# Optimization experiments

Measured on AMD Instinct MI355X. Metric: run time of the kernel, lower is better.

## Reference

```python
import jax, jax.numpy as jnp
import numpy as np

D_MODEL = 768
D_STATE = 16
D_CONV = 4
EXPAND = 2
D_INNER = EXPAND * D_MODEL
DT_RANK = (D_MODEL + 15) // 16  # 48
BATCH = 2
SEQ = 1024
LN_EPS = 1e-5


def setup_inputs() -> dict:
    key = jax.random.key(0)
    ks = jax.random.split(key, 12)
    s = 0.02
    inp = {
        "x": jax.random.normal(ks[0], (BATCH, SEQ, D_MODEL), dtype=jnp.float32),
        "in_proj_w": jax.random.normal(ks[1], (2 * D_INNER, D_MODEL), dtype=jnp.float32) * s,
        "conv_w": jax.random.normal(ks[2], (D_INNER, D_CONV), dtype=jnp.float32) * s,
        "conv_b": jnp.zeros((D_INNER,), dtype=jnp.float32),
        "x_proj_w": jax.random.normal(ks[3], (DT_RANK + 2 * D_STATE, D_INNER), dtype=jnp.float32) * s,
        "dt_proj_w": jax.random.normal(ks[4], (D_INNER, DT_RANK), dtype=jnp.float32) * s,
        "dt_proj_b": jnp.full((D_INNER,), -4.0, dtype=jnp.float32),  # softplus(-4) ~ small dt
        "A_log": jnp.log(jnp.broadcast_to(jnp.arange(1, D_STATE + 1, dtype=jnp.float32), (D_INNER, D_STATE))),
        "D": jnp.ones((D_INNER,), dtype=jnp.float32),
        "out_proj_w": jax.random.normal(ks[5], (D_MODEL, D_INNER), dtype=jnp.float32) * s,
        "ln_w": jnp.ones((D_MODEL,), dtype=jnp.float32),
        "ln_b": jnp.zeros((D_MODEL,), dtype=jnp.float32),
    }
    return inp


def _mamba(x, in_proj_w, conv_w, conv_b, x_proj_w, dt_proj_w, dt_proj_b, A_log, D, out_proj_w):
    B, L, _ = x.shape
    # input projection -> [B, L, 2*D_INNER], split into x-branch and gate z
    xz = jnp.einsum("bld,ed->ble", x, in_proj_w)
    xb, z = jnp.split(xz, 2, axis=-1)
    # causal depthwise conv1d along L
    lhs = jnp.transpose(xb, (0, 2, 1))  # [B, D_INNER, L]
    rhs = conv_w[:, None, :]  # [D_INNER, 1, D_CONV]
    xc = jax.lax.conv_general_dilated(
        lhs, rhs, window_strides=(1,), padding=[(D_CONV - 1, 0)],
        dimension_numbers=("NCH", "OIH", "NCH"), feature_group_count=D_INNER)
    xc = jnp.transpose(xc, (0, 2, 1)) + conv_b  # [B, L, D_INNER]
    xc = jax.nn.silu(xc)
    # data-dependent SSM parameters
    x_dbl = jnp.einsum("bld,ed->ble", xc, x_proj_w)  # [B, L, DT_RANK+2*D_STATE]
    dt, Bm, Cm = jnp.split(x_dbl, [DT_RANK, DT_RANK + D_STATE], axis=-1)
    dt = jax.nn.softplus(jnp.einsum("blr,dr->bld", dt, dt_proj_w) + dt_proj_b)  # [B, L, D_INNER]
    A = -jnp.exp(A_log)  # [D_INNER, D_STATE]

    # selective scan over time
    def step(h, inp):
        dt_t, B_t, C_t, u_t = inp  # [B,D_INNER], [B,D_STATE], [B,D_STATE], [B,D_INNER]
        dA = jnp.exp(dt_t[:, :, None] * A)  # [B, D_INNER, D_STATE]
        h = h * dA + (dt_t * u_t)[:, :, None] * B_t[:, None, :]
        y = jnp.einsum("bds,bs->bd", h, C_t)
        return h, y

    h0 = jnp.zeros((B, D_INNER, D_STATE), dtype=x.dtype)
    xs = (jnp.transpose(dt, (1, 0, 2)), jnp.transpose(Bm, (1, 0, 2)),
          jnp.transpose(Cm, (1, 0, 2)), jnp.transpose(xc, (1, 0, 2)))
    _, ys = jax.lax.scan(step, h0, xs)  # ys: [L, B, D_INNER]
    y = jnp.transpose(ys, (1, 0, 2)) + xc * D
    y = y * jax.nn.silu(z)
    return jnp.einsum("ble,de->bld", y, out_proj_w)  # [B, L, D_MODEL]


def reference(x, in_proj_w, conv_w, conv_b, x_proj_w, dt_proj_w, dt_proj_b,
              A_log, D, out_proj_w, ln_w, ln_b):
    residual = x
    h = _mamba(x, in_proj_w, conv_w, conv_b, x_proj_w, dt_proj_w, dt_proj_b, A_log, D, out_proj_w)
    # dropout is identity in eval mode
    y = h + residual
    mu = jnp.mean(y, axis=-1, keepdims=True)
    var = jnp.mean(jnp.square(y - mu), axis=-1, keepdims=True)
    return (y - mu) * jax.lax.rsqrt(var + LN_EPS) * ln_w + ln_b
```

## Files before the change

### kernel.cpp

```cpp
#include <hip/hip_runtime.h>
#include <hip/hip_bf16.h>
#include <math.h>

#define BATCH   2
#define SEQ     1024
#define DMODEL  768
#define DINNER  1536
#define DSTATE  16
#define DTRANK  48
#define NTOK    (BATCH*SEQ)
#define XPROJ_N (DTRANK + 2*DSTATE)

#define LC      32
#define NC      (SEQ/LC)

#define KSPL_IN   2
#define KSPL_OUT  4

typedef unsigned short ushort_t;
typedef __attribute__((ext_vector_type(8))) short bf16x8;
typedef __attribute__((ext_vector_type(4))) float f32x4;

__device__ __forceinline__ ushort_t f2bf(float f) {
    unsigned int u = __float_as_uint(f);
    u += 0x7FFF + ((u >> 16) & 1);
    return (ushort_t)(u >> 16);
}

__global__ __launch_bounds__(256)
void f2b_3(const float* __restrict__ s0, ushort_t* __restrict__ d0, int n0,
           const float* __restrict__ s1, ushort_t* __restrict__ d1, int n1,
           const float* __restrict__ s2, ushort_t* __restrict__ d2, int n2)
{
    const int i = (blockIdx.x * 256 + threadIdx.x) * 4;
    const float* s; ushort_t* d;
    if (i < n0)               { s = s0 + i;            d = d0 + i; }
    else if (i < n0 + n1)     { s = s1 + (i - n0);     d = d1 + (i - n0); }
    else if (i < n0 + n1 + n2){ s = s2 + (i - n0 - n1);d = d2 + (i - n0 - n1); }
    else return;
    const float4 v = *reinterpret_cast<const float4*>(s);
    ushort4 o;
    o.x = f2bf(v.x); o.y = f2bf(v.y); o.z = f2bf(v.z); o.w = f2bf(v.w);
    *reinterpret_cast<ushort4*>(d) = o;
}

#define GLOAD_LDS16(gp, lp) \
    __builtin_amdgcn_global_load_lds((const __attribute__((address_space(1))) void*)(gp), \
                                     (__attribute__((address_space(3))) void*)(lp), 16, 0, 0)

__global__ __launch_bounds__(256)
void gemm_mfma_bt_sk(const ushort_t* __restrict__ A, const ushort_t* __restrict__ W,
                     float* __restrict__ C, int M, int N, int K, int klen)
{
    __shared__ ushort_t As[128 * 32];
    __shared__ ushort_t Bs[128 * 32];

    const int tid  = threadIdx.x;
    const int w    = tid >> 6;
    const int lane = tid & 63;
    const int m0 = blockIdx.y * 128;
    const int n0 = blockIdx.x * 128;
    const int kbeg = blockIdx.z * klen;
    float* Cp = C + (size_t)blockIdx.z * M * N;

    const int lrow = lane >> 2;
    const int lcol = (lane & 3) * 8;

    const ushort_t* ga0 = A + (size_t)(m0 + w * 16 + lrow) * K + kbeg + lcol;
    const ushort_t* ga1 = ga0 + (size_t)64 * K;
    const ushort_t* gb0 = W + (size_t)(n0 + w * 16 + lrow) * K + kbeg + lcol;
    const ushort_t* gb1 = gb0 + (size_t)64 * K;

    ushort_t* lA0 = As + w * 512;
    ushort_t* lA1 = As + 64 * 32 + w * 512;
    ushort_t* lB0 = Bs + w * 512;
    ushort_t* lB1 = Bs + 64 * 32 + w * 512;

    const int wm = w >> 1, wn = w & 1;
    const int fr = lane & 15;
    const int kg = lane >> 4;

    f32x4 acc[4][4] = {};

    for (int kt = 0; kt < klen; kt += 32) {
        __syncthreads();
        GLOAD_LDS16(ga0 + kt, lA0);
        GLOAD_LDS16(ga1 + kt, lA1);
        GLOAD_LDS16(gb0 + kt, lB0);
        GLOAD_LDS16(gb1 + kt, lB1);
        __syncthreads();

        bf16x8 af[4], bfr[4];
        #pragma unroll
        for (int i = 0; i < 4; ++i) {
            af[i]  = *reinterpret_cast<const bf16x8*>(&As[(wm * 64 + i * 16 + fr) * 32 + kg * 8]);
            bfr[i] = *reinterpret_cast<const bf16x8*>(&Bs[(wn * 64 + i * 16 + fr) * 32 + kg * 8]);
        }
        #pragma unroll
        for (int i = 0; i < 4; ++i)
            #pragma unroll
            for (int j = 0; j < 4; ++j)
                acc[i][j] = __builtin_amdgcn_mfma_f32_16x16x32_bf16(af[i], bfr[j], acc[i][j], 0, 0, 0);
    }

    #pragma unroll
    for (int i = 0; i < 4; ++i) {
        const int row_base = m0 + wm * 64 + i * 16 + kg * 4;
        #pragma unroll
        for (int j = 0; j < 4; ++j) {
            const int col = n0 + wn * 64 + j * 16 + fr;
            #pragma unroll
            for (int r = 0; r < 4; ++r)
                Cp[(size_t)(row_base + r) * N + col] = acc[i][j][r];
        }
    }
}

#define BM 64
#define BN 64
#define BK 16

template<int ACT>
__global__ __launch_bounds__(256)
void gemm_tn(const float* __restrict__ A, const float* __restrict__ W,
             const float* __restrict__ bias, float* __restrict__ C,
             int M, int N, int K, int lda)
{
    __shared__ float As[BK][BM + 4];
    __shared__ float Ws[BK][BN + 4];

    const int t  = threadIdx.x;
    const int tx = t & 15;
    const int ty = t >> 4;
    const int row0 = blockIdx.y * BM;
    const int col0 = blockIdx.x * BN;

    const int m_l = t >> 2;
    const int k_l = (t & 3) * 4;

    float acc[4][4] = {};

    for (int kt = 0; kt < K; kt += BK) {
        float4 av, wv;
        {
            const float* ap = A + (size_t)(row0 + m_l) * lda + kt + k_l;
            av = *reinterpret_cast<const float4*>(ap);
        }
        {
            const int wn = col0 + m_l;
            if (wn < N) {
                const float* wp = W + (size_t)wn * K + kt + k_l;
                wv = *reinterpret_cast<const float4*>(wp);
            } else {
                wv = make_float4(0.f, 0.f, 0.f, 0.f);
            }
        }
        __syncthreads();
        As[k_l + 0][m_l] = av.x; As[k_l + 1][m_l] = av.y;
        As[k_l + 2][m_l] = av.z; As[k_l + 3][m_l] = av.w;
        Ws[k_l + 0][m_l] = wv.x; Ws[k_l + 1][m_l] = wv.y;
        Ws[k_l + 2][m_l] = wv.z; Ws[k_l + 3][m_l] = wv.w;
        __syncthreads();

        #pragma unroll
        for (int k = 0; k < BK; ++k) {
            float4 a4 = *reinterpret_cast<const float4*>(&As[k][ty * 4]);
            float4 w4 = *reinterpret_cast<const float4*>(&Ws[k][tx * 4]);
            float af[4] = {a4.x, a4.y, a4.z, a4.w};
            float wf[4] = {w4.x, w4.y, w4.z, w4.w};
            #pragma unroll
            for (int i = 0; i < 4; ++i)
                #pragma unroll
                for (int j = 0; j < 4; ++j)
                    acc[i][j] += af[i] * wf[j];
        }
    }

    #pragma unroll
    for (int i = 0; i < 4; ++i) {
        const int m = row0 + ty * 4 + i;
        #pragma unroll
        for (int j = 0; j < 4; ++j) {
            const int n = col0 + tx * 4 + j;
            if (n < N) {
                float v = acc[i][j];
                if (ACT == 1) {
                    v += bias[n];
                    v = (v > 20.f) ? v : log1pf(expf(v));
                }
                C[(size_t)m * N + n] = v;
            }
        }
    }
}

__global__ __launch_bounds__(256)
void gemm_tn_splitk(const float* __restrict__ A, const float* __restrict__ W,
                    float* __restrict__ C, int M, int N, int K, int lda, int kchunk)
{
    __shared__ float As[BK][BM + 4];
    __shared__ float Ws[BK][BN + 4];

    const int t  = threadIdx.x;
    const int tx = t & 15;
    const int ty = t >> 4;
    const int row0 = blockIdx.y * BM;
    const int col0 = blockIdx.x * BN;
    const int kbeg = blockIdx.z * kchunk;
    const int kend = kbeg + kchunk;

    const int m_l = t >> 2;
    const int k_l = (t & 3) * 4;

    float acc[4][4] = {};

    for (int kt = kbeg; kt < kend; kt += BK) {
        float4 av, wv;
        {
            const float* ap = A + (size_t)(row0 + m_l) * lda + kt + k_l;
            av = *reinterpret_cast<const float4*>(ap);
        }
        {
            const int wn = col0 + m_l;
            if (wn < N) {
                const float* wp = W + (size_t)wn * K + kt + k_l;
                wv = *reinterpret_cast<const float4*>(wp);
            } else {
                wv = make_float4(0.f, 0.f, 0.f, 0.f);
            }
        }
        __syncthreads();
        As[k_l + 0][m_l] = av.x; As[k_l + 1][m_l] = av.y;
        As[k_l + 2][m_l] = av.z; As[k_l + 3][m_l] = av.w;
        Ws[k_l + 0][m_l] = wv.x; Ws[k_l + 1][m_l] = wv.y;
        Ws[k_l + 2][m_l] = wv.z; Ws[k_l + 3][m_l] = wv.w;
        __syncthreads();

        #pragma unroll
        for (int k = 0; k < BK; ++k) {
            float4 a4 = *reinterpret_cast<const float4*>(&As[k][ty * 4]);
            float4 w4 = *reinterpret_cast<const float4*>(&Ws[k][tx * 4]);
            float af[4] = {a4.x, a4.y, a4.z, a4.w};
            float wf[4] = {w4.x, w4.y, w4.z, w4.w};
            #pragma unroll
            for (int i = 0; i < 4; ++i)
                #pragma unroll
                for (int j = 0; j < 4; ++j)
                    acc[i][j] += af[i] * wf[j];
        }
    }

    #pragma unroll
    for (int i = 0; i < 4; ++i) {
        const int m = row0 + ty * 4 + i;
        #pragma unroll
        for (int j = 0; j < 4; ++j) {
            const int n = col0 + tx * 4 + j;
            if (n < N)
                atomicAdd(&C[(size_t)m * N + n], acc[i][j]);
        }
    }
}

__global__ __launch_bounds__(256)
void conv_silu(const float* __restrict__ xzA, const float* __restrict__ xzB,
               const float* __restrict__ cw, const float* __restrict__ cb,
               float* __restrict__ xc)
{
    int idx = blockIdx.x * 256 + threadIdx.x;
    if (idx >= NTOK * DINNER) return;
    const int c = idx % DINNER;
    const int m = idx / DINNER;
    const int l = m & (SEQ - 1);

    const float w0 = cw[c * 4 + 0], w1 = cw[c * 4 + 1],
                w2 = cw[c * 4 + 2], w3 = cw[c * 4 + 3];
    const float* a = xzA + (size_t)m * (2 * DINNER) + c;
    const float* b = xzB + (size_t)m * (2 * DINNER) + c;
    const int R = 2 * DINNER;

    float acc = cb[c] + (a[0] + b[0]) * w3;
    if (l >= 1) acc += (a[-R]     + b[-R])     * w2;
    if (l >= 2) acc += (a[-2 * R] + b[-2 * R]) * w1;
    if (l >= 3) acc += (a[-3 * R] + b[-3 * R]) * w0;

    const float sig = 1.f / (1.f + __expf(-acc));
    xc[idx] = acc * sig;
}

__global__ __launch_bounds__(256)
void scan_chunk_state(const float* __restrict__ dt, const float* __restrict__ xc,
                      const float* __restrict__ xdbl, const float* __restrict__ A_log,
                      float* __restrict__ hA, float* __restrict__ aP)
{
    __shared__ float B_s[LC * 16];

    const int c  = blockIdx.x;
    const int d0 = blockIdx.y * 256;
    const int b  = blockIdx.z;
    const int t  = threadIdx.x;
    const int d  = d0 + t;

    const size_t row0 = (size_t)b * SEQ + (size_t)c * LC;

    #pragma unroll
    for (int p = 0; p < (LC * 16) / 256; ++p) {
        const int idx = p * 256 + t;
        const int l = idx >> 4, j = idx & 15;
        B_s[idx] = xdbl[(row0 + l) * XPROJ_N + DTRANK + j];
    }
    __syncthreads();

    float Aval[16];
    #pragma unroll
    for (int q = 0; q < 4; ++q) {
        const float4 a4 = *reinterpret_cast<const float4*>(&A_log[(size_t)d * DSTATE + q * 4]);
        Aval[q*4+0] = -expf(a4.x); Aval[q*4+1] = -expf(a4.y);
        Aval[q*4+2] = -expf(a4.z); Aval[q*4+3] = -expf(a4.w);
    }

    float h[16];
    #pragma unroll
    for (int s = 0; s < 16; ++s) h[s] = 0.f;
    float dts = 0.f;

    #pragma unroll 2
    for (int l = 0; l < LC; ++l) {
        const size_t m = row0 + l;
        const float dtv = dt[m * DINNER + d];
        const float u   = xc[m * DINNER + d];
        const float du  = dtv * u;
        dts += dtv;
        float Bv[16];
        #pragma unroll
        for (int q = 0; q < 4; ++q) {
            const float4 b4 = *reinterpret_cast<const float4*>(&B_s[l * 16 + q * 4]);
            Bv[q*4+0] = b4.x; Bv[q*4+1] = b4.y; Bv[q*4+2] = b4.z; Bv[q*4+3] = b4.w;
        }
        #pragma unroll
        for (int s = 0; s < 16; ++s)
            h[s] = h[s] * __expf(dtv * Aval[s]) + du * Bv[s];
    }

    const size_t o = (((size_t)(b * NC + c) * DINNER) + d) * DSTATE;
    #pragma unroll
    for (int q = 0; q < 4; ++q) {
        float4 hv = make_float4(h[q*4+0], h[q*4+1], h[q*4+2], h[q*4+3]);
        float4 pv = make_float4(__expf(Aval[q*4+0]*dts), __expf(Aval[q*4+1]*dts),
                                __expf(Aval[q*4+2]*dts), __expf(Aval[q*4+3]*dts));
        *reinterpret_cast<float4*>(&hA[o + q*4]) = hv;
        *reinterpret_cast<float4*>(&aP[o + q*4]) = pv;
    }
}

__global__ __launch_bounds__(256)
void scan_combine(float* __restrict__ hA, const float* __restrict__ aP)
{
    const int idx = blockIdx.x * 256 + threadIdx.x;
    const int b  = idx / (DINNER * DSTATE);
    const int ds = idx % (DINNER * DSTATE);

    float h = 0.f;
    #pragma unroll
    for (int c = 0; c < NC; ++c) {
        const size_t o = ((size_t)(b * NC + c) * DINNER * DSTATE) + ds;
        const float a = hA[o];
        const float p = aP[o];
        hA[o] = h;
        h = a + h * p;
    }
}

__global__ __launch_bounds__(256)
void scan_apply(const float* __restrict__ dt, const float* __restrict__ xc,
                const float* __restrict__ xdbl,
                const float* __restrict__ xzA, const float* __restrict__ xzB,
                const float* __restrict__ A_log, const float* __restrict__ Dp,
                const float* __restrict__ hInit, ushort_t* __restrict__ y)
{
    __shared__ float B_s[LC * 16];
    __shared__ float C_s[LC * 16];

    const int c  = blockIdx.x;
    const int d0 = blockIdx.y * 256;
    const int b  = blockIdx.z;
    const int t  = threadIdx.x;
    const int d  = d0 + t;

    const size_t row0 = (size_t)b * SEQ + (size_t)c * LC;

    #pragma unroll
    for (int p = 0; p < (LC * 16) / 256; ++p) {
        const int idx = p * 256 + t;
        const int l = idx >> 4, j = idx & 15;
        B_s[idx] = xdbl[(row0 + l) * XPROJ_N + DTRANK + j];
        C_s[idx] = xdbl[(row0 + l) * XPROJ_N + DTRANK + DSTATE + j];
    }
    __syncthreads();

    float Aval[16];
    #pragma unroll
    for (int q = 0; q < 4; ++q) {
        const float4 a4 = *reinterpret_cast<const float4*>(&A_log[(size_t)d * DSTATE + q * 4]);
        Aval[q*4+0] = -expf(a4.x); Aval[q*4+1] = -expf(a4.y);
        Aval[q*4+2] = -expf(a4.z); Aval[q*4+3] = -expf(a4.w);
    }
    const float Dd = Dp[d];

    const size_t o = (((size_t)(b * NC + c) * DINNER) + d) * DSTATE;
    float h[16];
    #pragma unroll
    for (int q = 0; q < 4; ++q) {
        const float4 h4 = *reinterpret_cast<const float4*>(&hInit[o + q*4]);
        h[q*4+0] = h4.x; h[q*4+1] = h4.y; h[q*4+2] = h4.z; h[q*4+3] = h4.w;
    }

    #pragma unroll 2
    for (int l = 0; l < LC; ++l) {
        const size_t m = row0 + l;
        const float dtv = dt[m * DINNER + d];
        const float u   = xc[m * DINNER + d];
        const size_t zi = m * (2 * DINNER) + DINNER + d;
        const float zv  = xzA[zi] + xzB[zi];
        const float du  = dtv * u;

        float acc = 0.f;
        #pragma unroll
        for (int q = 0; q < 4; ++q) {
            const float4 b4 = *reinterpret_cast<const float4*>(&B_s[l * 16 + q * 4]);
            const float4 c4 = *reinterpret_cast<const float4*>(&C_s[l * 16 + q * 4]);
            const float bb[4] = {b4.x, b4.y, b4.z, b4.w};
            const float cc[4] = {c4.x, c4.y, c4.z, c4.w};
            #pragma unroll
            for (int r = 0; r < 4; ++r) {
                const int s = q * 4 + r;
                h[s] = h[s] * __expf(dtv * Aval[s]) + du * bb[r];
                acc += h[s] * cc[r];
            }
        }

        const float yv  = acc + u * Dd;
        const float sig = 1.f / (1.f + __expf(-zv));
        y[m * DINNER + d] = f2bf(yv * zv * sig);
    }
}

__global__ __launch_bounds__(256)
void ln_kernel(const float* __restrict__ mo, const float* __restrict__ x,
               const float* __restrict__ w, const float* __restrict__ bias,
               float* __restrict__ out)
{
    const int m = blockIdx.x;
    const int t = threadIdx.x;
    const size_t MN = (size_t)NTOK * DMODEL;
    const float* mrow = mo + (size_t)m * DMODEL;
    const float* xrow = x  + (size_t)m * DMODEL;

    float v[3];
    float sum = 0.f, ss = 0.f;
    #pragma unroll
    for (int i = 0; i < 3; ++i) {
        const int col = t + 256 * i;
        float acc = xrow[col];
        #pragma unroll
        for (int p = 0; p < KSPL_OUT; ++p)
            acc += mrow[p * MN + col];
        v[i] = acc;
        sum += acc;
        ss  += acc * acc;
    }
    #pragma unroll
    for (int o = 1; o < 64; o <<= 1) {
        sum += __shfl_xor(sum, o);
        ss  += __shfl_xor(ss, o);
    }
    __shared__ float red[2][4];
    const int wid = t >> 6;
    if ((t & 63) == 0) { red[0][wid] = sum; red[1][wid] = ss; }
    __syncthreads();
    sum = red[0][0] + red[0][1] + red[0][2] + red[0][3];
    ss  = red[1][0] + red[1][1] + red[1][2] + red[1][3];

    const float mu   = sum * (1.f / DMODEL);
    const float var  = ss * (1.f / DMODEL) - mu * mu;
    const float rstd = rsqrtf(var + 1e-5f);

    #pragma unroll
    for (int i = 0; i < 3; ++i) {
        const int col = t + 256 * i;
        out[(size_t)m * DMODEL + col] = (v[i] - mu) * rstd * w[col] + bias[col];
    }
}

extern "C" void kernel_launch(void* const* d_in, const int* in_sizes, int n_in,
                              void* d_out, int out_size, void* d_ws, size_t ws_size,
                              hipStream_t stream)
{
    const float* x          = (const float*)d_in[0];
    const float* in_proj_w  = (const float*)d_in[1];
    const float* conv_w     = (const float*)d_in[2];
    const float* conv_b     = (const float*)d_in[3];
    const float* x_proj_w   = (const float*)d_in[4];
    const float* dt_proj_w  = (const float*)d_in[5];
    const float* dt_proj_b  = (const float*)d_in[6];
    const float* A_log      = (const float*)d_in[7];
    const float* Dp         = (const float*)d_in[8];
    const float* out_proj_w = (const float*)d_in[9];
    const float* ln_w       = (const float*)d_in[10];
    const float* ln_b       = (const float*)d_in[11];
    float* out = (float*)d_out;

    float* ws   = (float*)d_ws;
    float* xz   = ws;
    float* xc   = xz   + (size_t)KSPL_IN * NTOK * 3072;
    float* xdbl = xc   + (size_t)NTOK * 1536;
    float* dt   = xdbl + (size_t)NTOK * 80;
    float* mo   = dt   + (size_t)NTOK * 1536;
    ushort_t* xb16 = (ushort_t*)(mo + (size_t)KSPL_OUT * NTOK * 768);
    ushort_t* ipw16 = xb16  + (size_t)NTOK * DMODEL;
    ushort_t* opw16 = ipw16 + (size_t)2 * DINNER * DMODEL;
    ushort_t* ybb   = opw16 + (size_t)DMODEL * DINNER;

    float* xzA = xz;
    float* xzB = xz + (size_t)NTOK * 3072;

    float* aP = mo;
    float* hA = (float*)d_out;

    {
        const int n0 = NTOK * DMODEL;
        const int n1 = 2 * DINNER * DMODEL;
        const int n2 = DMODEL * DINNER;
        const int nvec = (n0 + n1 + n2) / 4;
        f2b_3<<<(nvec + 255) / 256, 256, 0, stream>>>(
            x, xb16, n0, in_proj_w, ipw16, n1, out_proj_w, opw16, n2);
    }

    gemm_mfma_bt_sk<<<dim3(2 * DINNER / 128, NTOK / 128, KSPL_IN), 256, 0, stream>>>(
        xb16, ipw16, xz, NTOK, 2 * DINNER, DMODEL, DMODEL / KSPL_IN);

    conv_silu<<<(NTOK * DINNER) / 256, 256, 0, stream>>>(xzA, xzB, conv_w, conv_b, xc);

    hipMemsetAsync(xdbl, 0, (size_t)NTOK * XPROJ_N * sizeof(float), stream);
    gemm_tn_splitk<<<dim3((XPROJ_N + BN - 1) / BN, NTOK / BM, 8), 256, 0, stream>>>(
        xc, x_proj_w, xdbl, NTOK, XPROJ_N, DINNER, DINNER, DINNER / 8);

    gemm_tn<1><<<dim3(DINNER / BN, NTOK / BM), 256, 0, stream>>>(
        xdbl, dt_proj_w, dt_proj_b, dt, NTOK, DINNER, DTRANK, XPROJ_N);

    scan_chunk_state<<<dim3(NC, DINNER / 256, BATCH), 256, 0, stream>>>(
        dt, xc, xdbl, A_log, hA, aP);
    scan_combine<<<(BATCH * DINNER * DSTATE) / 256, 256, 0, stream>>>(hA, aP);
    scan_apply<<<dim3(NC, DINNER / 256, BATCH), 256, 0, stream>>>(
        dt, xc, xdbl, xzA, xzB, A_log, Dp, hA, ybb);

    gemm_mfma_bt_sk<<<dim3(DMODEL / 128, NTOK / 128, KSPL_OUT), 256, 0, stream>>>(
        ybb, opw16, mo, NTOK, DMODEL, DINNER, DINNER / KSPL_OUT);

    ln_kernel<<<NTOK, 256, 0, stream>>>(mo, x, ln_w, ln_b, out);
}
```

Before: 257.1 us.

## Replace x_proj atomic split-K with partial buffers, vectorize conv and scan combine

```diff
diff --git a/kernel.cpp b/kernel.cpp
--- a/kernel.cpp
+++ b/kernel.cpp
@@ -10,12 +10,14 @@
 #define DTRANK  48
 #define NTOK    (BATCH*SEQ)
 #define XPROJ_N (DTRANK + 2*DSTATE)
+#define XP_PSZ  ((size_t)NTOK * XPROJ_N)
 
 #define LC      32
 #define NC      (SEQ/LC)
 
 #define KSPL_IN   2
 #define KSPL_OUT  4
+#define KSPL_XP   8
 
 typedef unsigned short ushort_t;
 typedef __attribute__((ext_vector_type(8))) short bf16x8;
@@ -120,27 +122,31 @@
 #define BN 64
 #define BK 16
 
-template<int ACT>
-__global__ __launch_bounds__(256)
-void gemm_tn(const float* __restrict__ A, const float* __restrict__ W,
-             const float* __restrict__ bias, float* __restrict__ C,
-             int M, int N, int K, int lda)
+__global__ __launch_bounds__(256)
+void gemm_tn_xp(const float* __restrict__ A, const float* __restrict__ W,
+                float* __restrict__ C)
 {
     __shared__ float As[BK][BM + 4];
     __shared__ float Ws[BK][BN + 4];
+
+    const int M = NTOK, N = XPROJ_N, K = DINNER, lda = DINNER;
+    const int kchunk = DINNER / KSPL_XP;
 
     const int t  = threadIdx.x;
     const int tx = t & 15;
     const int ty = t >> 4;
     const int row0 = blockIdx.y * BM;
     const int col0 = blockIdx.x * BN;
+    const int kbeg = blockIdx.z * kchunk;
+    const int kend = kbeg + kchunk;
+    float* Cp = C + (size_t)blockIdx.z * XP_PSZ;
 
     const int m_l = t >> 2;
     const int k_l = (t & 3) * 4;
 
     float acc[4][4] = {};
 
-    for (int kt = 0; kt < K; kt += BK) {
+    for (int kt = kbeg; kt < kend; kt += BK) {
         float4 av, wv;
         {
             const float* ap = A + (size_t)(row0 + m_l) * lda + kt + k_l;
@@ -182,52 +188,47 @@
         #pragma unroll
         for (int j = 0; j < 4; ++j) {
             const int n = col0 + tx * 4 + j;
-            if (n < N) {
-                float v = acc[i][j];
-                if (ACT == 1) {
-                    v += bias[n];
-                    v = (v > 20.f) ? v : log1pf(expf(v));
-                }
-                C[(size_t)m * N + n] = v;
-            }
-        }
-    }
-}
-
-__global__ __launch_bounds__(256)
-void gemm_tn_splitk(const float* __restrict__ A, const float* __restrict__ W,
-                    float* __restrict__ C, int M, int N, int K, int lda, int kchunk)
+            if (n < N)
+                Cp[(size_t)m * N + n] = acc[i][j];
+        }
+    }
+}
+
+__global__ __launch_bounds__(256)
+void gemm_tn_dt(const float* __restrict__ Ap, const float* __restrict__ W,
+                const float* __restrict__ bias, float* __restrict__ C)
 {
     __shared__ float As[BK][BM + 4];
     __shared__ float Ws[BK][BN + 4];
+
+    const int N = DINNER, K = DTRANK, lda = XPROJ_N;
 
     const int t  = threadIdx.x;
     const int tx = t & 15;
     const int ty = t >> 4;
     const int row0 = blockIdx.y * BM;
     const int col0 = blockIdx.x * BN;
-    const int kbeg = blockIdx.z * kchunk;
-    const int kend = kbeg + kchunk;
 
     const int m_l = t >> 2;
     const int k_l = (t & 3) * 4;
 
     float acc[4][4] = {};
 
-    for (int kt = kbeg; kt < kend; kt += BK) {
-        float4 av, wv;
+    for (int kt = 0; kt < K; kt += BK) {
+        float4 av = make_float4(0.f, 0.f, 0.f, 0.f);
         {
-            const float* ap = A + (size_t)(row0 + m_l) * lda + kt + k_l;
-            av = *reinterpret_cast<const float4*>(ap);
-        }
+            const size_t off = (size_t)(row0 + m_l) * lda + kt + k_l;
+            #pragma unroll
+            for (int p = 0; p < KSPL_XP; ++p) {
+                const float4 v = *reinterpret_cast<const float4*>(Ap + p * XP_PSZ + off);
+                av.x += v.x; av.y += v.y; av.z += v.z; av.w += v.w;
+            }
+        }
+        float4 wv;
         {
             const int wn = col0 + m_l;
-            if (wn < N) {
-                const float* wp = W + (size_t)wn * K + kt + k_l;
-                wv = *reinterpret_cast<const float4*>(wp);
-            } else {
-                wv = make_float4(0.f, 0.f, 0.f, 0.f);
-            }
+            const float* wp = W + (size_t)wn * K + kt + k_l;
+            wv = *reinterpret_cast<const float4*>(wp);
         }
         __syncthreads();
         As[k_l + 0][m_l] = av.x; As[k_l + 1][m_l] = av.y;
@@ -256,8 +257,9 @@
         #pragma unroll
         for (int j = 0; j < 4; ++j) {
             const int n = col0 + tx * 4 + j;
-            if (n < N)
-                atomicAdd(&C[(size_t)m * N + n], acc[i][j]);
+            float v = acc[i][j] + bias[n];
+            v = (v > 20.f) ? v : log1pf(expf(v));
+            C[(size_t)m * N + n] = v;
         }
     }
 }
@@ -267,30 +269,61 @@
                const float* __restrict__ cw, const float* __restrict__ cb,
                float* __restrict__ xc)
 {
-    int idx = blockIdx.x * 256 + threadIdx.x;
-    if (idx >= NTOK * DINNER) return;
-    const int c = idx % DINNER;
-    const int m = idx / DINNER;
-    const int l = m & (SEQ - 1);
-
-    const float w0 = cw[c * 4 + 0], w1 = cw[c * 4 + 1],
-                w2 = cw[c * 4 + 2], w3 = cw[c * 4 + 3];
-    const float* a = xzA + (size_t)m * (2 * DINNER) + c;
-    const float* b = xzB + (size_t)m * (2 * DINNER) + c;
-    const int R = 2 * DINNER;
-
-    float acc = cb[c] + (a[0] + b[0]) * w3;
-    if (l >= 1) acc += (a[-R]     + b[-R])     * w2;
-    if (l >= 2) acc += (a[-2 * R] + b[-2 * R]) * w1;
-    if (l >= 3) acc += (a[-3 * R] + b[-3 * R]) * w0;
-
-    const float sig = 1.f / (1.f + __expf(-acc));
-    xc[idx] = acc * sig;
+    const int vid = blockIdx.x * 256 + threadIdx.x;
+    const int c4 = (vid % (DINNER / 4)) * 4;
+    const int m  = vid / (DINNER / 4);
+    const int l  = m & (SEQ - 1);
+    const int R  = 2 * DINNER;
+
+    const float* a = xzA + (size_t)m * R + c4;
+    const float* b = xzB + (size_t)m * R + c4;
+
+    float4 W0 = *reinterpret_cast<const float4*>(cw + (c4 + 0) * 4);
+    float4 W1 = *reinterpret_cast<const float4*>(cw + (c4 + 1) * 4);
+    float4 W2 = *reinterpret_cast<const float4*>(cw + (c4 + 2) * 4);
+    float4 W3 = *reinterpret_cast<const float4*>(cw + (c4 + 3) * 4);
+    const float4 bias = *reinterpret_cast<const float4*>(cb + c4);
+
+    float4 s0 = *reinterpret_cast<const float4*>(a);
+    {
+        const float4 t = *reinterpret_cast<const float4*>(b);
+        s0.x += t.x; s0.y += t.y; s0.z += t.z; s0.w += t.w;
+    }
+    float acc0 = bias.x + s0.x * W0.w;
+    float acc1 = bias.y + s0.y * W1.w;
+    float acc2 = bias.z + s0.z * W2.w;
+    float acc3 = bias.w + s0.w * W3.w;
+
+    if (l >= 1) {
+        float4 s = *reinterpret_cast<const float4*>(a - R);
+        const float4 t = *reinterpret_cast<const float4*>(b - R);
+        s.x += t.x; s.y += t.y; s.z += t.z; s.w += t.w;
+        acc0 += s.x * W0.z; acc1 += s.y * W1.z; acc2 += s.z * W2.z; acc3 += s.w * W3.z;
+    }
+    if (l >= 2) {
+        float4 s = *reinterpret_cast<const float4*>(a - 2 * R);
+        const float4 t = *reinterpret_cast<const float4*>(b - 2 * R);
+        s.x += t.x; s.y += t.y; s.z += t.z; s.w += t.w;
+        acc0 += s.x * W0.y; acc1 += s.y * W1.y; acc2 += s.z * W2.y; acc3 += s.w * W3.y;
+    }
+    if (l >= 3) {
+        float4 s = *reinterpret_cast<const float4*>(a - 3 * R);
+        const float4 t = *reinterpret_cast<const float4*>(b - 3 * R);
+        s.x += t.x; s.y += t.y; s.z += t.z; s.w += t.w;
+        acc0 += s.x * W0.x; acc1 += s.y * W1.x; acc2 += s.z * W2.x; acc3 += s.w * W3.x;
+    }
+
+    float4 o;
+    o.x = acc0 / (1.f + __expf(-acc0));
+    o.y = acc1 / (1.f + __expf(-acc1));
+    o.z = acc2 / (1.f + __expf(-acc2));
+    o.w = acc3 / (1.f + __expf(-acc3));
+    *reinterpret_cast<float4*>(xc + (size_t)m * DINNER + c4) = o;
 }
 
 __global__ __launch_bounds__(256)
 void scan_chunk_state(const float* __restrict__ dt, const float* __restrict__ xc,
-                      const float* __restrict__ xdbl, const float* __restrict__ A_log,
+                      const float* __restrict__ xdblP, const float* __restrict__ A_log,
                       float* __restrict__ hA, float* __restrict__ aP)
 {
     __shared__ float B_s[LC * 16];
@@ -307,7 +340,11 @@
     for (int p = 0; p < (LC * 16) / 256; ++p) {
         const int idx = p * 256 + t;
         const int l = idx >> 4, j = idx & 15;
-        B_s[idx] = xdbl[(row0 + l) * XPROJ_N + DTRANK + j];
+        const size_t off = (row0 + l) * XPROJ_N + DTRANK + j;
+        float v = 0.f;
+        #pragma unroll
+        for (int q = 0; q < KSPL_XP; ++q) v += xdblP[q * XP_PSZ + off];
+        B_s[idx] = v;
     }
     __syncthreads();
 
@@ -359,21 +396,27 @@
     const int idx = blockIdx.x * 256 + threadIdx.x;
     const int b  = idx / (DINNER * DSTATE);
     const int ds = idx % (DINNER * DSTATE);
-
+    const size_t stride = (size_t)DINNER * DSTATE;
+    const size_t base = (size_t)b * NC * stride + ds;
+
+    float a[NC], p[NC];
+    #pragma unroll
+    for (int c = 0; c < NC; ++c) {
+        a[c] = hA[base + (size_t)c * stride];
+        p[c] = aP[base + (size_t)c * stride];
+    }
     float h = 0.f;
     #pragma unroll
     for (int c = 0; c < NC; ++c) {
-        const size_t o = ((size_t)(b * NC + c) * DINNER * DSTATE) + ds;
-        const float a = hA[o];
-        const float p = aP[o];
-        hA[o] = h;
-        h = a + h * p;
+        const float hn = a[c] + h * p[c];
+        hA[base + (size_t)c * stride] = h;
+        h = hn;
     }
 }
 
 __global__ __launch_bounds__(256)
 void scan_apply(const float* __restrict__ dt, const float* __restrict__ xc,
-                const float* __restrict__ xdbl,
+                const float* __restrict__ xdblP,
                 const float* __restrict__ xzA, const float* __restrict__ xzB,
                 const float* __restrict__ A_log, const float* __restrict__ Dp,
                 const float* __restrict__ hInit, ushort_t* __restrict__ y)
@@ -393,8 +436,15 @@
     for (int p = 0; p < (LC * 16) / 256; ++p) {
         const int idx = p * 256 + t;
         const int l = idx >> 4, j = idx & 15;
-        B_s[idx] = xdbl[(row0 + l) * XPROJ_N + DTRANK + j];
-        C_s[idx] = xdbl[(row0 + l) * XPROJ_N + DTRANK + DSTATE + j];
+        const size_t offB = (row0 + l) * XPROJ_N + DTRANK + j;
+        float vb = 0.f, vc = 0.f;
+        #pragma unroll
+        for (int q = 0; q < KSPL_XP; ++q) {
+            vb += xdblP[q * XP_PSZ + offB];
+            vc += xdblP[q * XP_PSZ + offB + DSTATE];
+        }
+        B_s[idx] = vb;
+        C_s[idx] = vc;
     }
     __syncthreads();
 
@@ -514,7 +564,7 @@
     float* xz   = ws;
     float* xc   = xz   + (size_t)KSPL_IN * NTOK * 3072;
     float* xdbl = xc   + (size_t)NTOK * 1536;
-    float* dt   = xdbl + (size_t)NTOK * 80;
+    float* dt   = xdbl + (size_t)KSPL_XP * XP_PSZ;
     float* mo   = dt   + (size_t)NTOK * 1536;
     ushort_t* xb16 = (ushort_t*)(mo + (size_t)KSPL_OUT * NTOK * 768);
     ushort_t* ipw16 = xb16  + (size_t)NTOK * DMODEL;
@@ -539,14 +589,13 @@
     gemm_mfma_bt_sk<<<dim3(2 * DINNER / 128, NTOK / 128, KSPL_IN), 256, 0, stream>>>(
         xb16, ipw16, xz, NTOK, 2 * DINNER, DMODEL, DMODEL / KSPL_IN);
 
-    conv_silu<<<(NTOK * DINNER) / 256, 256, 0, stream>>>(xzA, xzB, conv_w, conv_b, xc);
-
-    hipMemsetAsync(xdbl, 0, (size_t)NTOK * XPROJ_N * sizeof(float), stream);
-    gemm_tn_splitk<<<dim3((XPROJ_N + BN - 1) / BN, NTOK / BM, 8), 256, 0, stream>>>(
-        xc, x_proj_w, xdbl, NTOK, XPROJ_N, DINNER, DINNER, DINNER / 8);
-
-    gemm_tn<1><<<dim3(DINNER / BN, NTOK / BM), 256, 0, stream>>>(
-        xdbl, dt_proj_w, dt_proj_b, dt, NTOK, DINNER, DTRANK, XPROJ_N);
+    conv_silu<<<(NTOK * DINNER / 4) / 256, 256, 0, stream>>>(xzA, xzB, conv_w, conv_b, xc);
+
+    gemm_tn_xp<<<dim3((XPROJ_N + BN - 1) / BN, NTOK / BM, KSPL_XP), 256, 0, stream>>>(
+        xc, x_proj_w, xdbl);
+
+    gemm_tn_dt<<<dim3(DINNER / BN, NTOK / BM), 256, 0, stream>>>(
+        xdbl, dt_proj_w, dt_proj_b, dt);
 
     scan_chunk_state<<<dim3(NC, DINNER / 256, BATCH), 256, 0, stream>>>(
         dt, xc, xdbl, A_log, hA, aP);
```

Result: faster. 244.2 us (-5.0%).
